# Optimization experiments

Measured on AMD Instinct MI355X. Metric: run time of the kernel, lower is better.

Reference implementation:

```python
import jax, jax.numpy as jnp
import numpy as np

LN_EPS = 1e-5

def setup_inputs() -> dict:
    key = jax.random.key(0)
    ks = jax.random.split(key, 16)
    B, N = 16384, 1000000
    return {
        "user_input": jax.random.randint(ks[0], (B,), 0, N),
        "emb": jax.random.normal(ks[1], (N, 64), jnp.float32),
        "sc_country_idx": jax.random.randint(ks[2], (N,), 0, 256),
        "sc_country_emb": jax.random.normal(ks[3], (256, 32), jnp.float32),
        "sc_device_idx": jax.random.randint(ks[4], (N,), 0, 10000),
        "sc_device_emb": jax.random.normal(ks[5], (10000, 32), jnp.float32),
        "mf_tags_idx": jax.random.randint(ks[6], (N, 20), 0, 50000),
        "mf_tags_emb": jax.random.normal(ks[7], (50000, 32), jnp.float32),
        "mf_history_idx": jax.random.randint(ks[8], (N, 50), 0, 100000),
        "mf_history_emb": jax.random.normal(ks[9], (100000, 32), jnp.float32),
        "fc_w": jax.random.normal(ks[10], (256, 192), jnp.float32) * 0.05,
        "fc_b": jax.random.normal(ks[11], (256,), jnp.float32) * 0.05,
        "ln_g": jnp.ones((256,), jnp.float32),
        "ln_b": jnp.zeros((256,), jnp.float32),
    }

def _layernorm(x, g, b):
    mu = jnp.mean(x, axis=-1, keepdims=True)
    var = jnp.mean(jnp.square(x - mu), axis=-1, keepdims=True)
    return (x - mu) * jax.lax.rsqrt(var + LN_EPS) * g + b

def reference(user_input, emb, sc_country_idx, sc_country_emb, sc_device_idx, sc_device_emb,
               mf_tags_idx, mf_tags_emb, mf_history_idx, mf_history_emb,
               fc_w, fc_b, ln_g, ln_b):
    parts = [emb[user_input]]  # [B, 64]
    # scalar side features: buffer lookup then embedding gather -> [B, 32]
    parts.append(sc_country_emb[sc_country_idx[user_input]])
    parts.append(sc_device_emb[sc_device_idx[user_input]])
    # multi-valued side features: [B, W] index lists -> gather -> mean pool -> [B, 32]
    parts.append(jnp.mean(mf_tags_emb[mf_tags_idx[user_input]], axis=1))
    parts.append(jnp.mean(mf_history_emb[mf_history_idx[user_input]], axis=1))
    x = jnp.concatenate(parts, axis=-1)  # [B, 192]
    x = jax.nn.relu(x @ fc_w.T + fc_b)   # [B, 256]
    return _layernorm(x, ln_g, ln_b)
```

## Files before the change

### kernel.cpp

```cpp
#include <hip/hip_runtime.h>

#define LN_EPS 1e-5f

typedef _Float16 f16;
typedef _Float16 f16x4 __attribute__((ext_vector_type(4)));
typedef _Float16 f16x8 __attribute__((ext_vector_type(8)));
typedef float    f32x4 __attribute__((ext_vector_type(4)));

constexpr int KDIM = 192;
constexpr int NOUT = 256;

__global__ __launch_bounds__(256)
void ut_wconv_kernel(const float* __restrict__ fc_w, f16* __restrict__ W16)
{
    const int i = blockIdx.x * 256 + threadIdx.x;
    const float4 v = ((const float4*)fc_w)[i];
    f16x4 h = { (f16)v.x, (f16)v.y, (f16)v.z, (f16)v.w };
    ((f16x4*)W16)[i] = h;
}

__global__ __launch_bounds__(256)
void ut_gather_kernel(const int*   __restrict__ user_input,
                      const float* __restrict__ emb,
                      const int*   __restrict__ sc_country_idx,
                      const float* __restrict__ sc_country_emb,
                      const int*   __restrict__ sc_device_idx,
                      const float* __restrict__ sc_device_emb,
                      const int*   __restrict__ mf_tags_idx,
                      const float* __restrict__ mf_tags_emb,
                      const int*   __restrict__ mf_history_idx,
                      const float* __restrict__ mf_history_emb,
                      f16*         __restrict__ X16,
                      int B)
{
    const int lane = threadIdx.x & 63;
    const int wave = threadIdx.x >> 6;
    const int row  = blockIdx.x * 4 + wave;
    if (row >= B) return;

    const int half = lane >> 5;
    const int col  = lane & 31;
    const int jt   = lane >> 3;
    const int fc   = lane & 7;

    const int u = __builtin_amdgcn_readfirstlane(user_input[row]);
    f16* __restrict__ Xr = X16 + (size_t)row * KDIM;

    const int ci = sc_country_idx[u];
    const int di = sc_device_idx[u];

    const int* __restrict__ tp = mf_tags_idx    + (size_t)u * 20;
    const int* __restrict__ hp = mf_history_idx + (size_t)u * 50;

    int  ti[3];  bool tv[3];
    #pragma unroll
    for (int p = 0; p < 3; ++p) {
        const int j = p * 8 + jt;
        tv[p] = (j < 20);
        ti[p] = tv[p] ? tp[j] : 0;
    }
    int  hi[7];  bool hv[7];
    #pragma unroll
    for (int p = 0; p < 7; ++p) {
        const int j = p * 8 + jt;
        hv[p] = (j < 50);
        hi[p] = hv[p] ? hp[j] : 0;
    }

    const float e = emb[(size_t)u * 64 + lane];

    const float sc = (half == 0) ? sc_country_emb[ci * 32 + col]
                                 : sc_device_emb [di * 32 + col];

    float4 ta4 = make_float4(0.f, 0.f, 0.f, 0.f);
    #pragma unroll
    for (int p = 0; p < 3; ++p) {
        const float4 g = *(const float4*)&mf_tags_emb[(size_t)ti[p] * 32 + fc * 4];
        if (tv[p]) { ta4.x += g.x; ta4.y += g.y; ta4.z += g.z; ta4.w += g.w; }
    }
    float4 ha4 = make_float4(0.f, 0.f, 0.f, 0.f);
    #pragma unroll
    for (int p = 0; p < 7; ++p) {
        const float4 g = *(const float4*)&mf_history_emb[(size_t)hi[p] * 32 + fc * 4];
        if (hv[p]) { ha4.x += g.x; ha4.y += g.y; ha4.z += g.z; ha4.w += g.w; }
    }

    #pragma unroll
    for (int m = 8; m <= 32; m <<= 1) {
        ta4.x += __shfl_xor(ta4.x, m, 64);  ta4.y += __shfl_xor(ta4.y, m, 64);
        ta4.z += __shfl_xor(ta4.z, m, 64);  ta4.w += __shfl_xor(ta4.w, m, 64);
        ha4.x += __shfl_xor(ha4.x, m, 64);  ha4.y += __shfl_xor(ha4.y, m, 64);
        ha4.z += __shfl_xor(ha4.z, m, 64);  ha4.w += __shfl_xor(ha4.w, m, 64);
    }

    Xr[lane] = (f16)e;
    if (half == 0) Xr[64 + col] = (f16)sc;
    else           Xr[96 + col] = (f16)sc;
    if (lane < 8) {
        const float s_t = 1.f / 20.f, s_h = 1.f / 50.f;
        f16x4 t = { (f16)(ta4.x * s_t), (f16)(ta4.y * s_t),
                    (f16)(ta4.z * s_t), (f16)(ta4.w * s_t) };
        f16x4 h = { (f16)(ha4.x * s_h), (f16)(ha4.y * s_h),
                    (f16)(ha4.z * s_h), (f16)(ha4.w * s_h) };
        *(f16x4*)&Xr[128 + lane * 4] = t;
        *(f16x4*)&Xr[160 + lane * 4] = h;
    }
}

__global__ __launch_bounds__(256)
void ut_fc_ln_kernel(const f16*   __restrict__ X16,
                     const f16*   __restrict__ W16,
                     const float* __restrict__ fc_b,
                     const float* __restrict__ ln_g,
                     const float* __restrict__ ln_b,
                     float*       __restrict__ out,
                     int B)
{
    __shared__ float sb[4][16];
    __shared__ float s2b[4][16];

    const int tid  = threadIdx.x;
    const int lane = tid & 63;
    const int wave = tid >> 6;
    const int t    = lane & 15;
    const int quad = lane >> 4;
    const int row0 = blockIdx.x * 16;
    if (row0 >= B) return;
    const int colbase = wave * 64;

    const f16* __restrict__ arow = X16 + (size_t)(row0 + t) * KDIM + quad * 8;

    f32x4 acc[4];
    #pragma unroll
    for (int ct = 0; ct < 4; ++ct) acc[ct] = (f32x4){0.f, 0.f, 0.f, 0.f};

    #pragma unroll
    for (int kt = 0; kt < 6; ++kt) {
        const f16x8 a = *(const f16x8*)(arow + kt * 32);
        #pragma unroll
        for (int ct = 0; ct < 4; ++ct) {
            const f16x8 b = *(const f16x8*)(W16 + (size_t)(colbase + ct * 16 + t) * KDIM
                                                 + kt * 32 + quad * 8);
            acc[ct] = __builtin_amdgcn_mfma_f32_16x16x32_f16(a, b, acc[ct], 0, 0, 0);
        }
    }

    float bias[4], g4[4], bb4[4];
    #pragma unroll
    for (int ct = 0; ct < 4; ++ct) {
        const int c = colbase + ct * 16 + t;
        bias[ct] = fc_b[c];
        g4[ct]   = ln_g[c];
        bb4[ct]  = ln_b[c];
    }

    float y[4][4];
    float s[4]  = {0.f, 0.f, 0.f, 0.f};
    float s2[4] = {0.f, 0.f, 0.f, 0.f};
    #pragma unroll
    for (int ct = 0; ct < 4; ++ct) {
        #pragma unroll
        for (int r = 0; r < 4; ++r) {
            const float v = fmaxf(acc[ct][r] + bias[ct], 0.f);
            y[ct][r] = v;
            s[r]  += v;
            s2[r] += v * v;
        }
    }
    #pragma unroll
    for (int m = 1; m <= 8; m <<= 1) {
        #pragma unroll
        for (int r = 0; r < 4; ++r) {
            s[r]  += __shfl_xor(s[r],  m, 64);
            s2[r] += __shfl_xor(s2[r], m, 64);
        }
    }
    if (t == 0) {
        #pragma unroll
        for (int r = 0; r < 4; ++r) {
            sb [wave][quad * 4 + r] = s[r];
            s2b[wave][quad * 4 + r] = s2[r];
        }
    }
    __syncthreads();

    #pragma unroll
    for (int r = 0; r < 4; ++r) {
        const int rho = quad * 4 + r;
        const float st  = sb [0][rho] + sb [1][rho] + sb [2][rho] + sb [3][rho];
        const float s2t = s2b[0][rho] + s2b[1][rho] + s2b[2][rho] + s2b[3][rho];
        const float mu  = st  * (1.f / 256.f);
        const float var = s2t * (1.f / 256.f) - mu * mu;
        const float rs  = rsqrtf(var + LN_EPS);
        #pragma unroll
        for (int ct = 0; ct < 4; ++ct) {
            const int c = colbase + ct * 16 + t;
            out[(size_t)(row0 + rho) * NOUT + c] = (y[ct][r] - mu) * rs * g4[ct] + bb4[ct];
        }
    }
}

extern "C" void kernel_launch(void* const* d_in, const int* in_sizes, int n_in,
                              void* d_out, int out_size, void* d_ws, size_t ws_size,
                              hipStream_t stream)
{
    const int*   user_input     = (const int*)  d_in[0];
    const float* emb            = (const float*)d_in[1];
    const int*   sc_country_idx = (const int*)  d_in[2];
    const float* sc_country_emb = (const float*)d_in[3];
    const int*   sc_device_idx  = (const int*)  d_in[4];
    const float* sc_device_emb  = (const float*)d_in[5];
    const int*   mf_tags_idx    = (const int*)  d_in[6];
    const float* mf_tags_emb    = (const float*)d_in[7];
    const int*   mf_history_idx = (const int*)  d_in[8];
    const float* mf_history_emb = (const float*)d_in[9];
    const float* fc_w           = (const float*)d_in[10];
    const float* fc_b           = (const float*)d_in[11];
    const float* ln_g           = (const float*)d_in[12];
    const float* ln_b           = (const float*)d_in[13];
    float*       out            = (float*)d_out;

    f16* X16 = (f16*)d_ws;
    f16* W16 = (f16*)((char*)d_ws + (size_t)(16 << 20));

    const int B = in_sizes[0];

    ut_wconv_kernel<<<48, 256, 0, stream>>>(fc_w, W16);

    const int gatherGrid = (B + 3) / 4;
    ut_gather_kernel<<<gatherGrid, 256, 0, stream>>>(
        user_input, emb, sc_country_idx, sc_country_emb,
        sc_device_idx, sc_device_emb, mf_tags_idx, mf_tags_emb,
        mf_history_idx, mf_history_emb, X16, B);

    const int fcGrid = (B + 15) / 16;
    ut_fc_ln_kernel<<<fcGrid, 256, 0, stream>>>(
        X16, W16, fc_b, ln_g, ln_b, out, B);
}
```

Measured before the change: 464.2 us.

## Fuse embedding gather into FC+LayerNorm kernel via shared-memory staging

Merges the gather kernel and the FC+LayerNorm kernel into one. Each block gathers its 16 rows into a padded shared-memory tile, then runs the MFMA matmul and LayerNorm from that tile. This removes the global round trip of the fp16 intermediate and one kernel launch. In exchange each wave now handles four rows one after another, so the gather latency per block may be less overlapped, and the grid has fewer blocks.

After: 463.2 us. No clear change (-0.2%).

```diff
diff --git a/kernel.cpp b/kernel.cpp
--- a/kernel.cpp
+++ b/kernel.cpp
@@ -9,6 +9,7 @@
 
 constexpr int KDIM = 192;
 constexpr int NOUT = 256;
+constexpr int XSTR = 200;
 
 __global__ __launch_bounds__(256)
 void ut_wconv_kernel(const float* __restrict__ fc_w, f16* __restrict__ W16)
@@ -20,95 +21,16 @@
 }
 
 __global__ __launch_bounds__(256)
-void ut_gather_kernel(const int*   __restrict__ user_input,
-                      const float* __restrict__ emb,
-                      const int*   __restrict__ sc_country_idx,
-                      const float* __restrict__ sc_country_emb,
-                      const int*   __restrict__ sc_device_idx,
-                      const float* __restrict__ sc_device_emb,
-                      const int*   __restrict__ mf_tags_idx,
-                      const float* __restrict__ mf_tags_emb,
-                      const int*   __restrict__ mf_history_idx,
-                      const float* __restrict__ mf_history_emb,
-                      f16*         __restrict__ X16,
-                      int B)
-{
-    const int lane = threadIdx.x & 63;
-    const int wave = threadIdx.x >> 6;
-    const int row  = blockIdx.x * 4 + wave;
-    if (row >= B) return;
-
-    const int half = lane >> 5;
-    const int col  = lane & 31;
-    const int jt   = lane >> 3;
-    const int fc   = lane & 7;
-
-    const int u = __builtin_amdgcn_readfirstlane(user_input[row]);
-    f16* __restrict__ Xr = X16 + (size_t)row * KDIM;
-
-    const int ci = sc_country_idx[u];
-    const int di = sc_device_idx[u];
-
-    const int* __restrict__ tp = mf_tags_idx    + (size_t)u * 20;
-    const int* __restrict__ hp = mf_history_idx + (size_t)u * 50;
-
-    int  ti[3];  bool tv[3];
-    #pragma unroll
-    for (int p = 0; p < 3; ++p) {
-        const int j = p * 8 + jt;
-        tv[p] = (j < 20);
-        ti[p] = tv[p] ? tp[j] : 0;
-    }
-    int  hi[7];  bool hv[7];
-    #pragma unroll
-    for (int p = 0; p < 7; ++p) {
-        const int j = p * 8 + jt;
-        hv[p] = (j < 50);
-        hi[p] = hv[p] ? hp[j] : 0;
-    }
-
-    const float e = emb[(size_t)u * 64 + lane];
-
-    const float sc = (half == 0) ? sc_country_emb[ci * 32 + col]
-                                 : sc_device_emb [di * 32 + col];
-
-    float4 ta4 = make_float4(0.f, 0.f, 0.f, 0.f);
-    #pragma unroll
-    for (int p = 0; p < 3; ++p) {
-        const float4 g = *(const float4*)&mf_tags_emb[(size_t)ti[p] * 32 + fc * 4];
-        if (tv[p]) { ta4.x += g.x; ta4.y += g.y; ta4.z += g.z; ta4.w += g.w; }
-    }
-    float4 ha4 = make_float4(0.f, 0.f, 0.f, 0.f);
-    #pragma unroll
-    for (int p = 0; p < 7; ++p) {
-        const float4 g = *(const float4*)&mf_history_emb[(size_t)hi[p] * 32 + fc * 4];
-        if (hv[p]) { ha4.x += g.x; ha4.y += g.y; ha4.z += g.z; ha4.w += g.w; }
-    }
-
-    #pragma unroll
-    for (int m = 8; m <= 32; m <<= 1) {
-        ta4.x += __shfl_xor(ta4.x, m, 64);  ta4.y += __shfl_xor(ta4.y, m, 64);
-        ta4.z += __shfl_xor(ta4.z, m, 64);  ta4.w += __shfl_xor(ta4.w, m, 64);
-        ha4.x += __shfl_xor(ha4.x, m, 64);  ha4.y += __shfl_xor(ha4.y, m, 64);
-        ha4.z += __shfl_xor(ha4.z, m, 64);  ha4.w += __shfl_xor(ha4.w, m, 64);
-    }
-
-    Xr[lane] = (f16)e;
-    if (half == 0) Xr[64 + col] = (f16)sc;
-    else           Xr[96 + col] = (f16)sc;
-    if (lane < 8) {
-        const float s_t = 1.f / 20.f, s_h = 1.f / 50.f;
-        f16x4 t = { (f16)(ta4.x * s_t), (f16)(ta4.y * s_t),
-                    (f16)(ta4.z * s_t), (f16)(ta4.w * s_t) };
-        f16x4 h = { (f16)(ha4.x * s_h), (f16)(ha4.y * s_h),
-                    (f16)(ha4.z * s_h), (f16)(ha4.w * s_h) };
-        *(f16x4*)&Xr[128 + lane * 4] = t;
-        *(f16x4*)&Xr[160 + lane * 4] = h;
-    }
-}
-
-__global__ __launch_bounds__(256)
-void ut_fc_ln_kernel(const f16*   __restrict__ X16,
+void ut_fused_kernel(const int*   __restrict__ user_input,
+                     const float* __restrict__ emb,
+                     const int*   __restrict__ sc_country_idx,
+                     const float* __restrict__ sc_country_emb,
+                     const int*   __restrict__ sc_device_idx,
+                     const float* __restrict__ sc_device_emb,
+                     const int*   __restrict__ mf_tags_idx,
+                     const float* __restrict__ mf_tags_emb,
+                     const int*   __restrict__ mf_history_idx,
+                     const float* __restrict__ mf_history_emb,
                      const f16*   __restrict__ W16,
                      const float* __restrict__ fc_b,
                      const float* __restrict__ ln_g,
@@ -116,27 +38,101 @@
                      float*       __restrict__ out,
                      int B)
 {
+    __shared__ f16   Xs[16][XSTR];
     __shared__ float sb[4][16];
     __shared__ float s2b[4][16];
 
     const int tid  = threadIdx.x;
     const int lane = tid & 63;
     const int wave = tid >> 6;
+    const int row0 = blockIdx.x * 16;
+
+    const int half = lane >> 5;
+    const int col  = lane & 31;
+    const int jt   = lane >> 3;
+    const int fc   = lane & 7;
+
+    #pragma unroll
+    for (int rr = 0; rr < 4; ++rr) {
+        const int r16 = wave * 4 + rr;
+        const int row = row0 + r16;
+        if (row < B) {
+            const int u = __builtin_amdgcn_readfirstlane(user_input[row]);
+
+            const int ci = sc_country_idx[u];
+            const int di = sc_device_idx[u];
+
+            const int* __restrict__ tp = mf_tags_idx    + (size_t)u * 20;
+            const int* __restrict__ hp = mf_history_idx + (size_t)u * 50;
+
+            int  ti[3];  bool tv[3];
+            #pragma unroll
+            for (int p = 0; p < 3; ++p) {
+                const int j = p * 8 + jt;
+                tv[p] = (j < 20);
+                ti[p] = tv[p] ? tp[j] : 0;
+            }
+            int  hi[7];  bool hv[7];
+            #pragma unroll
+            for (int p = 0; p < 7; ++p) {
+                const int j = p * 8 + jt;
+                hv[p] = (j < 50);
+                hi[p] = hv[p] ? hp[j] : 0;
+            }
+
+            const float e = emb[(size_t)u * 64 + lane];
+
+            const float sc = (half == 0) ? sc_country_emb[ci * 32 + col]
+                                         : sc_device_emb [di * 32 + col];
+
+            float4 ta4 = make_float4(0.f, 0.f, 0.f, 0.f);
+            #pragma unroll
+            for (int p = 0; p < 3; ++p) {
+                const float4 g = *(const float4*)&mf_tags_emb[(size_t)ti[p] * 32 + fc * 4];
+                if (tv[p]) { ta4.x += g.x; ta4.y += g.y; ta4.z += g.z; ta4.w += g.w; }
+            }
+            float4 ha4 = make_float4(0.f, 0.f, 0.f, 0.f);
+            #pragma unroll
+            for (int p = 0; p < 7; ++p) {
+                const float4 g = *(const float4*)&mf_history_emb[(size_t)hi[p] * 32 + fc * 4];
+                if (hv[p]) { ha4.x += g.x; ha4.y += g.y; ha4.z += g.z; ha4.w += g.w; }
+            }
+
+            #pragma unroll
+            for (int m = 8; m <= 32; m <<= 1) {
+                ta4.x += __shfl_xor(ta4.x, m, 64);  ta4.y += __shfl_xor(ta4.y, m, 64);
+                ta4.z += __shfl_xor(ta4.z, m, 64);  ta4.w += __shfl_xor(ta4.w, m, 64);
+                ha4.x += __shfl_xor(ha4.x, m, 64);  ha4.y += __shfl_xor(ha4.y, m, 64);
+                ha4.z += __shfl_xor(ha4.z, m, 64);  ha4.w += __shfl_xor(ha4.w, m, 64);
+            }
+
+            Xs[r16][lane] = (f16)e;
+            if (half == 0) Xs[r16][64 + col] = (f16)sc;
+            else           Xs[r16][96 + col] = (f16)sc;
+            if (lane < 8) {
+                const float s_t = 1.f / 20.f, s_h = 1.f / 50.f;
+                f16x4 tq = { (f16)(ta4.x * s_t), (f16)(ta4.y * s_t),
+                             (f16)(ta4.z * s_t), (f16)(ta4.w * s_t) };
+                f16x4 hq = { (f16)(ha4.x * s_h), (f16)(ha4.y * s_h),
+                             (f16)(ha4.z * s_h), (f16)(ha4.w * s_h) };
+                *(f16x4*)&Xs[r16][128 + lane * 4] = tq;
+                *(f16x4*)&Xs[r16][160 + lane * 4] = hq;
+            }
+        }
+    }
+    __syncthreads();
+
     const int t    = lane & 15;
     const int quad = lane >> 4;
-    const int row0 = blockIdx.x * 16;
-    if (row0 >= B) return;
     const int colbase = wave * 64;
 
-    const f16* __restrict__ arow = X16 + (size_t)(row0 + t) * KDIM + quad * 8;
-
     f32x4 acc[4];
     #pragma unroll
     for (int ct = 0; ct < 4; ++ct) acc[ct] = (f32x4){0.f, 0.f, 0.f, 0.f};
 
     #pragma unroll
     for (int kt = 0; kt < 6; ++kt) {
-        const f16x8 a = *(const f16x8*)(arow + kt * 32);
+        const f16x8 a = *(const f16x8*)&Xs[t][kt * 32 + quad * 8];
         #pragma unroll
         for (int ct = 0; ct < 4; ++ct) {
             const f16x8 b = *(const f16x8*)(W16 + (size_t)(colbase + ct * 16 + t) * KDIM
@@ -192,10 +188,12 @@
         const float mu  = st  * (1.f / 256.f);
         const float var = s2t * (1.f / 256.f) - mu * mu;
         const float rs  = rsqrtf(var + LN_EPS);
-        #pragma unroll
-        for (int ct = 0; ct < 4; ++ct) {
-            const int c = colbase + ct * 16 + t;
-            out[(size_t)(row0 + rho) * NOUT + c] = (y[ct][r] - mu) * rs * g4[ct] + bb4[ct];
+        if (row0 + rho < B) {
+            #pragma unroll
+            for (int ct = 0; ct < 4; ++ct) {
+                const int c = colbase + ct * 16 + t;
+                out[(size_t)(row0 + rho) * NOUT + c] = (y[ct][r] - mu) * rs * g4[ct] + bb4[ct];
+            }
         }
     }
 }
@@ -220,20 +218,15 @@
     const float* ln_b           = (const float*)d_in[13];
     float*       out            = (float*)d_out;
 
-    f16* X16 = (f16*)d_ws;
-    f16* W16 = (f16*)((char*)d_ws + (size_t)(16 << 20));
+    f16* W16 = (f16*)d_ws;
 
     const int B = in_sizes[0];
 
     ut_wconv_kernel<<<48, 256, 0, stream>>>(fc_w, W16);
 
-    const int gatherGrid = (B + 3) / 4;
-    ut_gather_kernel<<<gatherGrid, 256, 0, stream>>>(
+    const int grid = (B + 15) / 16;
+    ut_fused_kernel<<<grid, 256, 0, stream>>>(
         user_input, emb, sc_country_idx, sc_country_emb,
         sc_device_idx, sc_device_emb, mf_tags_idx, mf_tags_emb,
-        mf_history_idx, mf_history_emb, X16, B);
-
-    const int fcGrid = (B + 15) / 16;
-    ut_fc_ln_kernel<<<fcGrid, 256, 0, stream>>>(
-        X16, W16, fc_b, ln_g, ln_b, out, B);
+        mf_history_idx, mf_history_emb, W16, fc_b, ln_g, ln_b, out, B);
 }
```
